# Kernel optimization log

Hardware: AMD Instinct MI355X
Metric: run time of the kernel (lower is better)

## Reference

```python
import jax, jax.numpy as jnp
import numpy as np

TEMPERATURE = 0.07
NEG_INF = -9e15
EPS = 1e-8  # matches torch F.cosine_similarity eps default


def setup_inputs() -> dict:
    key = jax.random.key(0)
    k1, k2 = jax.random.split(key)
    N, D = 4096, 512
    z1 = jax.random.normal(k1, (N, D), dtype=jnp.float32)
    z2 = jax.random.normal(k2, (N, D), dtype=jnp.float32)
    return {"z1": z1, "z2": z2}


def reference(z1, z2):
    N = z1.shape[0]
    z = jnp.concatenate([z1, z2], axis=0)  # [2N, D]
    # cosine similarity as normalized GEMM (torch clamps norm by eps)
    norm = jnp.maximum(jnp.linalg.norm(z, axis=-1, keepdims=True), EPS)
    zn = z / norm
    sim = (zn @ zn.T) / TEMPERATURE  # [2N, 2N]
    two_n = 2 * N
    idx = jnp.arange(two_n)
    sim = sim.at[idx, idx].set(NEG_INF)
    # positives: diag(sim, N) then diag(sim, -N)
    pos_upper = sim[idx[:N], idx[:N] + N]
    pos_lower = sim[idx[:N] + N, idx[:N]]
    positives = jnp.concatenate([pos_upper, pos_lower], axis=0)  # [2N]
    loss = -positives + jax.scipy.special.logsumexp(sim, axis=1)
    return loss.mean()
```

## Files before the change

kernel.cpp:

```cpp
#include <hip/hip_runtime.h>
#include <hip/hip_bf16.h>
#include <hip/hip_fp8.h>

#define N_ROWS 4096
#define TWO_N 8192
#define DIM 512
#define BKB 64
#define NKS (DIM / BKB)
#define INV_T 14.285714285714286f
#define LOG2E 1.4426950408889634f
#define C_LOG2E 20.60992915555662f
#define INV_SQRT_T 3.7796447300922722f

typedef float f32x4 __attribute__((ext_vector_type(4)));
typedef long fp8x8;

#define ASYNC_COPY16(gp, lp)                                                     \
  __builtin_amdgcn_global_load_lds((const __attribute__((address_space(1))) void*)(gp), \
                                   (__attribute__((address_space(3))) void*)(lp), 16, 0, 0)

#define VMCNT(n) asm volatile("s_waitcnt vmcnt(" #n ")" ::: "memory")

__global__ __launch_bounds__(256) void k_prep(const float* __restrict__ z1,
                                              const float* __restrict__ z2,
                                              unsigned char* __restrict__ zn,
                                              float* __restrict__ posbuf,
                                              float* __restrict__ rowsum) {
  const int t = threadIdx.x;
  const int wv = t >> 6, lane = t & 63;
  const int r = blockIdx.x * 4 + wv;
  if (blockIdx.x < 32) rowsum[blockIdx.x * 256 + t] = 0.f;

  const float4* p1 = reinterpret_cast<const float4*>(z1 + (size_t)r * DIM) + (lane << 1);
  const float4* p2 = reinterpret_cast<const float4*>(z2 + (size_t)r * DIM) + (lane << 1);
  float4 a0 = p1[0], a1 = p1[1];
  float4 b0 = p2[0], b1 = p2[1];

  float s1 = a0.x * a0.x + a0.y * a0.y + a0.z * a0.z + a0.w * a0.w
           + a1.x * a1.x + a1.y * a1.y + a1.z * a1.z + a1.w * a1.w;
  float s2 = b0.x * b0.x + b0.y * b0.y + b0.z * b0.z + b0.w * b0.w
           + b1.x * b1.x + b1.y * b1.y + b1.z * b1.z + b1.w * b1.w;
  float sd = a0.x * b0.x + a0.y * b0.y + a0.z * b0.z + a0.w * b0.w
           + a1.x * b1.x + a1.y * b1.y + a1.z * b1.z + a1.w * b1.w;
#pragma unroll
  for (int off = 1; off < 64; off <<= 1) {
    s1 += __shfl_xor(s1, off, 64);
    s2 += __shfl_xor(s2, off, 64);
    sd += __shfl_xor(sd, off, 64);
  }
  const float sc1 = INV_SQRT_T / fmaxf(sqrtf(s1), 1e-8f);
  const float sc2 = INV_SQRT_T / fmaxf(sqrtf(s2), 1e-8f);

  float va[8] = {a0.x, a0.y, a0.z, a0.w, a1.x, a1.y, a1.z, a1.w};
  float vb[8] = {b0.x, b0.y, b0.z, b0.w, b1.x, b1.y, b1.z, b1.w};
  unsigned long long pa = 0, pb = 0;
#pragma unroll
  for (int d = 0; d < 8; d++) {
    __hip_fp8_e4m3 qa(va[d] * sc1);
    __hip_fp8_e4m3 qb(vb[d] * sc2);
    pa |= (unsigned long long)qa.__x << (8 * d);
    pb |= (unsigned long long)qb.__x << (8 * d);
  }
  *reinterpret_cast<unsigned long long*>(zn + (size_t)r * DIM + lane * 8) = pa;
  *reinterpret_cast<unsigned long long*>(zn + (size_t)(r + N_ROWS) * DIM + lane * 8) = pb;

  if (lane == 0) posbuf[r] = sd * sc1 * sc2;
}

__global__ __launch_bounds__(256, 3) void k_lse(const unsigned char* __restrict__ Zn,
                                                float* __restrict__ rowsum) {
  __shared__ char smem[49152] __attribute__((aligned(16)));
  const int tid  = threadIdx.x;
  const int wave = tid >> 6;
  const int lane = tid & 63;
  const int cl   = lane & 15;
  const int q    = lane >> 4;

  const int b = (blockIdx.x & 7) * 260 + (blockIdx.x >> 3);

  int rt = (int)((129.0f - sqrtf(16641.0f - 8.0f * (float)b)) * 0.5f);
  if (rt > 63) rt = 63;
  if (rt < 0) rt = 0;
  while (rt > 0 && 64 * rt - rt * (rt - 1) / 2 > b) rt--;
  while (64 * (rt + 1) - (rt + 1) * rt / 2 <= b) rt++;
  const int ct = rt + (b - (64 * rt - rt * (rt - 1) / 2));

  const int wr = (wave >> 1) * 64;
  const int wc = (wave & 1) * 64;

  const int r0  = tid >> 2;
  const int kg0 = ((tid & 3) ^ (r0 & 3) ^ ((r0 >> 2) & 3)) * 16;
  const unsigned char* gA0 = Zn + (size_t)(rt * 128 + r0) * DIM + kg0;
  const unsigned char* gB0 = Zn + (size_t)(ct * 128 + r0) * DIM + kg0;

  f32x4 acc[4][4] = {};
  const int xk = (cl & 3) ^ (cl >> 2);
  const int qh = q >> 1;
  const int qb = (q & 1) * 8;

#define STAGE(d, it)                                                        \
  {                                                                         \
    char* _b = smem + (d) * 16384 + wave * 1024;                            \
    const int _ko = (it) * BKB;                                             \
    ASYNC_COPY16(gA0 + _ko,            _b);                                 \
    ASYNC_COPY16(gA0 + _ko + 64 * DIM, _b + 4096);                          \
    ASYNC_COPY16(gB0 + _ko,            _b + 8192);                          \
    ASYNC_COPY16(gB0 + _ko + 64 * DIM, _b + 12288);                         \
  }

  STAGE(0, 0);
  STAGE(1, 1);
#pragma unroll
  for (int ks = 0; ks < NKS; ks++) {
    const int cur = ks % 3;
    if (ks + 1 < NKS) { VMCNT(4); } else { VMCNT(0); }
    __builtin_amdgcn_s_barrier();
    asm volatile("" ::: "memory");
    if (ks + 2 < NKS) STAGE((ks + 2) % 3, ks + 2);

    const char* sA = smem + cur * 16384;
    const char* sB = sA + 8192;
    fp8x8 af[2][4], bfr[2][4];
#pragma unroll
    for (int ksub = 0; ksub < 2; ksub++) {
      const int gsl = (((ksub << 1) | qh) ^ xk) * 16 + qb;
#pragma unroll
      for (int i = 0; i < 4; i++)
        af[ksub][i] = *reinterpret_cast<const fp8x8*>(sA + (wr + i * 16 + cl) * 64 + gsl);
#pragma unroll
      for (int j = 0; j < 4; j++)
        bfr[ksub][j] = *reinterpret_cast<const fp8x8*>(sB + (wc + j * 16 + cl) * 64 + gsl);
    }
#pragma unroll
    for (int ksub = 0; ksub < 2; ksub++)
#pragma unroll
      for (int i = 0; i < 4; i++)
#pragma unroll
        for (int j = 0; j < 4; j++)
          acc[i][j] = __builtin_amdgcn_mfma_f32_16x16x32_fp8_fp8(af[ksub][i], bfr[ksub][j],
                                                                 acc[i][j], 0, 0, 0);
  }
#undef STAGE

  const bool diagw = (rt == ct) && (wr == wc);
  float psum[4][4];
#pragma unroll
  for (int i = 0; i < 4; i++)
#pragma unroll
    for (int r = 0; r < 4; r++) psum[i][r] = 0.f;
  float colp[4] = {0.f, 0.f, 0.f, 0.f};

#pragma unroll
  for (int i = 0; i < 4; i++)
#pragma unroll
    for (int j = 0; j < 4; j++)
#pragma unroll
      for (int r = 0; r < 4; r++) {
        float e = exp2f(fmaf(acc[i][j][r], LOG2E, -C_LOG2E));
        if (diagw && (i == j) && (cl == q * 4 + r)) e = 0.f;
        psum[i][r] += e;
        colp[j] += e;
      }

#pragma unroll
  for (int i = 0; i < 4; i++)
#pragma unroll
    for (int r = 0; r < 4; r++) {
      float v = psum[i][r];
      v += __shfl_xor(v, 1, 64);
      v += __shfl_xor(v, 2, 64);
      v += __shfl_xor(v, 4, 64);
      v += __shfl_xor(v, 8, 64);
      if (cl == 0) atomicAdd(&rowsum[rt * 128 + wr + i * 16 + q * 4 + r], v);
    }

  if (rt != ct) {
#pragma unroll
    for (int j = 0; j < 4; j++) {
      float v = colp[j];
      v += __shfl_xor(v, 16, 64);
      v += __shfl_xor(v, 32, 64);
      if (q == 0) atomicAdd(&rowsum[ct * 128 + wc + j * 16 + cl], v);
    }
  }
}

__global__ void k_final(const float* __restrict__ rowsum, const float* __restrict__ posbuf,
                        float* __restrict__ out) {
  __shared__ float red[16];
  const int t = threadIdx.x;
  float s = 0.f;
#pragma unroll
  for (int it = 0; it < TWO_N / 1024; it++) {
    const int row = it * 1024 + t;
    float v = logf(rowsum[row]);
    if (row < N_ROWS) v -= 2.f * posbuf[row];
    s += v;
  }
#pragma unroll
  for (int off = 32; off > 0; off >>= 1) s += __shfl_down(s, off, 64);
  if ((t & 63) == 0) red[t >> 6] = s;
  __syncthreads();
  if (t == 0) {
    float tot = 0.f;
#pragma unroll
    for (int i = 0; i < 16; i++) tot += red[i];
    out[0] = tot / (float)TWO_N + INV_T;
  }
}

extern "C" void kernel_launch(void* const* d_in, const int* in_sizes, int n_in,
                              void* d_out, int out_size, void* d_ws, size_t ws_size,
                              hipStream_t stream) {
  const float* z1 = (const float*)d_in[0];
  const float* z2 = (const float*)d_in[1];
  float* out = (float*)d_out;
  char* ws = (char*)d_ws;

  unsigned char* zn = (unsigned char*)ws;
  float* rowsum = (float*)(ws + 4194304);
  float* posbuf = (float*)(ws + 4227072);

  k_prep<<<1024, 256, 0, stream>>>(z1, z2, zn, posbuf, rowsum);
  k_lse<<<2080, 256, 0, stream>>>(zn, rowsum);
  k_final<<<1, 1024, 0, stream>>>(rowsum, posbuf, out);
}
```

Before: 121.9 us.

## Permute fp8 K layout in prep so LDS fragment reads become 16-byte loads

The prep kernel now stores each row's fp8 values in a permuted order within each 64-byte K block, interleaving the two k-subslices a lane needs. The GEMM kernel uses a matching swizzle, so each lane reads one 16-byte vector from LDS per row fragment instead of two 8-byte reads. This halves the number of LDS read instructions in the main loop. The risk is different bank-conflict behaviour under the new swizzle, and the permutation must match the MFMA k-ordering on both operands to stay correct.

Result: faster. 117.9 us (-3.3%).

```diff
diff --git a/kernel.cpp b/kernel.cpp
--- a/kernel.cpp
+++ b/kernel.cpp
@@ -14,6 +14,7 @@
 
 typedef float f32x4 __attribute__((ext_vector_type(4)));
 typedef long fp8x8;
+typedef long fp8x8x2 __attribute__((ext_vector_type(2)));
 
 #define ASYNC_COPY16(gp, lp)                                                     \
   __builtin_amdgcn_global_load_lds((const __attribute__((address_space(1))) void*)(gp), \
@@ -61,8 +62,9 @@
     pa |= (unsigned long long)qa.__x << (8 * d);
     pb |= (unsigned long long)qb.__x << (8 * d);
   }
-  *reinterpret_cast<unsigned long long*>(zn + (size_t)r * DIM + lane * 8) = pa;
-  *reinterpret_cast<unsigned long long*>(zn + (size_t)(r + N_ROWS) * DIM + lane * 8) = pb;
+  const int pofs = (lane >> 3) * 64 + (lane & 3) * 16 + ((lane >> 2) & 1) * 8;
+  *reinterpret_cast<unsigned long long*>(zn + (size_t)r * DIM + pofs) = pa;
+  *reinterpret_cast<unsigned long long*>(zn + (size_t)(r + N_ROWS) * DIM + pofs) = pb;
 
   if (lane == 0) posbuf[r] = sd * sc1 * sc2;
 }
@@ -89,14 +91,13 @@
   const int wc = (wave & 1) * 64;
 
   const int r0  = tid >> 2;
-  const int kg0 = ((tid & 3) ^ (r0 & 3) ^ ((r0 >> 2) & 3)) * 16;
-  const unsigned char* gA0 = Zn + (size_t)(rt * 128 + r0) * DIM + kg0;
-  const unsigned char* gB0 = Zn + (size_t)(ct * 128 + r0) * DIM + kg0;
+  const int sg  = ((tid & 3) ^ ((r0 >> 1) & 3)) * 16;
+  const unsigned char* gA0 = Zn + (size_t)(rt * 128 + r0) * DIM + sg;
+  const unsigned char* gB0 = Zn + (size_t)(ct * 128 + r0) * DIM + sg;
 
   f32x4 acc[4][4] = {};
-  const int xk = (cl & 3) ^ (cl >> 2);
-  const int qh = q >> 1;
-  const int qb = (q & 1) * 8;
+  const int xk2 = (cl >> 1) & 3;
+  const int gofs = ((q ^ xk2) << 4);
 
 #define STAGE(d, it)                                                        \
   {                                                                         \
@@ -122,14 +123,16 @@
     const char* sB = sA + 8192;
     fp8x8 af[2][4], bfr[2][4];
 #pragma unroll
-    for (int ksub = 0; ksub < 2; ksub++) {
-      const int gsl = (((ksub << 1) | qh) ^ xk) * 16 + qb;
-#pragma unroll
-      for (int i = 0; i < 4; i++)
-        af[ksub][i] = *reinterpret_cast<const fp8x8*>(sA + (wr + i * 16 + cl) * 64 + gsl);
-#pragma unroll
-      for (int j = 0; j < 4; j++)
-        bfr[ksub][j] = *reinterpret_cast<const fp8x8*>(sB + (wc + j * 16 + cl) * 64 + gsl);
+    for (int i = 0; i < 4; i++) {
+      fp8x8x2 av = *reinterpret_cast<const fp8x8x2*>(sA + (wr + i * 16 + cl) * 64 + gofs);
+      af[0][i] = av[0];
+      af[1][i] = av[1];
+    }
+#pragma unroll
+    for (int j = 0; j < 4; j++) {
+      fp8x8x2 bv = *reinterpret_cast<const fp8x8x2*>(sB + (wc + j * 16 + cl) * 64 + gofs);
+      bfr[0][j] = bv[0];
+      bfr[1][j] = bv[1];
     }
 #pragma unroll
     for (int ksub = 0; ksub < 2; ksub++)
```
